# Optimization experiments

Measured on AMD Instinct MI355X. Metric: run time of the kernel, lower is better.

Reference implementation:

```python
import jax, jax.numpy as jnp
import numpy as np

N_NODES = 100000
N_EDGES = 3200000
D_IN = 96      # sum(latent_dim)
D_OUT = 32     # latent_dim[-1]
N_HEADS = 4
LEAKY_SLOPE = 0.2


def setup_inputs() -> dict:
    key = jax.random.key(0)
    k_x, k_w, k_a, k_src, k_dst = jax.random.split(key, 5)
    x = jax.random.normal(k_x, (N_NODES, D_IN), dtype=jnp.float32)
    # per-head GAT params (xavier-ish scale)
    W = jax.random.normal(k_w, (N_HEADS, D_IN, D_OUT), dtype=jnp.float32) * (1.414 / np.sqrt(D_IN))
    a = jax.random.normal(k_a, (N_HEADS, 2 * D_OUT), dtype=jnp.float32) * 0.1
    edge_src = jax.random.randint(k_src, (N_EDGES,), 0, N_NODES)
    edge_dst = jax.random.randint(k_dst, (N_EDGES,), 0, N_NODES)
    return {"x": x, "W": W, "a": a, "edge_src": edge_src, "edge_dst": edge_dst}


def reference(x, W, a, edge_src, edge_dst):
    # Multi-head sparse GAT layer (SpGraphAttentionLayer, concat=True, eval mode).
    N = x.shape[0]
    n_heads, _, d_out = W.shape
    outs = []
    for i in range(n_heads):  # small fixed head loop; data dims fully vectorized
        h = x @ W[i]                                   # [N, d_out]
        # a @ cat(h[src], h[dst]) == h[src]@a1 + h[dst]@a2 (avoids [E, 2*d_out] concat)
        s = h[edge_src] @ a[i, :d_out] + h[edge_dst] @ a[i, d_out:]   # [E]
        edge_e = jnp.exp(-jax.nn.leaky_relu(s, LEAKY_SLOPE))          # [E]
        # sparse_coo(edge, edge_e, [N,N]) @ h  ==  scatter-add of edge_e * h[dst] into src
        msg = edge_e[:, None] * h[edge_dst]                           # [E, d_out]
        h_prime = jax.ops.segment_sum(msg, edge_src, num_segments=N)  # [N, d_out]
        outs.append(jax.nn.elu(h_prime))
    return jnp.concatenate(outs, axis=1)  # [N, n_heads * d_out]
```

## Files before the change

kernel.cpp:

```cpp
#include <hip/hip_runtime.h>
#include <hip/hip_bf16.h>

#define DIN 96
#define DOUT 32
#define NH 4
#define DTOT 128
#define SLOPE 0.2f
#define NPBF 64
#define BSH 7
#define BNODES 128
#define MAXB 1024
#define EPB 4096
#define BCAP 5632
#define QSL  2304
#define SLSZ 2432

__device__ __forceinline__ unsigned int packbf2(float lo, float hi) {
    unsigned int a = __float_as_uint(lo), b = __float_as_uint(hi);
    a += 0x7fffu + ((a >> 16) & 1u);
    b += 0x7fffu + ((b >> 16) & 1u);
    return (a >> 16) | (b & 0xffff0000u);
}

__global__ __launch_bounds__(256) void feat_kernel(
    const float* __restrict__ x, const float* __restrict__ W,
    const float* __restrict__ a,
    unsigned int* __restrict__ hq,
    float2* __restrict__ usrc, float2* __restrict__ vdst,
    int n_nodes)
{
    __shared__ float Wlo[DIN * 64];
    __shared__ float Whi[DIN * 64];
    __shared__ float al[NH * 2 * DOUT];
    const int t = threadIdx.x;

    for (int i = t; i < DIN * DTOT; i += 256) {
        int k = i >> 7, c = i & 127;
        int head = c >> 5, j = c & 31;
        float w = W[head * (DIN * DOUT) + k * DOUT + j];
        int cbi = c >> 3, jj = c & 7;
        if (jj < 4) Wlo[(k << 6) + (cbi << 2) + jj] = w;
        else        Whi[(k << 6) + (cbi << 2) + (jj - 4)] = w;
    }
    for (int i = t; i < NH * 2 * DOUT; i += 256) al[i] = a[i];
    __syncthreads();

    const int cbi = t & 15;
    const int ng = t >> 4;
    const int node0 = blockIdx.x * NPBF;
    const int g0 = node0 + ng * 4;

    bool ok[4];
    const float* xp[4];
#pragma unroll
    for (int i = 0; i < 4; ++i) {
        ok[i] = (g0 + i) < n_nodes;
        xp[i] = x + (size_t)(g0 + i) * DIN;
    }

    float acc[4][8];
#pragma unroll
    for (int i = 0; i < 4; ++i)
#pragma unroll
        for (int j = 0; j < 8; ++j) acc[i][j] = 0.f;

    for (int k = 0; k < DIN; k += 4) {
        float4 xv[4];
#pragma unroll
        for (int i = 0; i < 4; ++i)
            xv[i] = ok[i] ? *(const float4*)(xp[i] + k)
                          : make_float4(0.f, 0.f, 0.f, 0.f);
#pragma unroll
        for (int kk = 0; kk < 4; ++kk) {
            const float4 wlo = *(const float4*)&Wlo[((k + kk) << 6) + (cbi << 2)];
            const float4 whi = *(const float4*)&Whi[((k + kk) << 6) + (cbi << 2)];
#pragma unroll
            for (int i = 0; i < 4; ++i) {
                const float xvv = (kk == 0) ? xv[i].x : (kk == 1) ? xv[i].y
                                 : (kk == 2) ? xv[i].z : xv[i].w;
                acc[i][0] = fmaf(xvv, wlo.x, acc[i][0]);
                acc[i][1] = fmaf(xvv, wlo.y, acc[i][1]);
                acc[i][2] = fmaf(xvv, wlo.z, acc[i][2]);
                acc[i][3] = fmaf(xvv, wlo.w, acc[i][3]);
                acc[i][4] = fmaf(xvv, whi.x, acc[i][4]);
                acc[i][5] = fmaf(xvv, whi.y, acc[i][5]);
                acc[i][6] = fmaf(xvv, whi.z, acc[i][6]);
                acc[i][7] = fmaf(xvv, whi.w, acc[i][7]);
            }
        }
    }

    const int head = cbi >> 2;
    const int j0 = (cbi & 3) << 3;
#pragma unroll
    for (int i = 0; i < 4; ++i) {
        float ps = 0.f, pd = 0.f;
#pragma unroll
        for (int j = 0; j < 8; ++j) {
            ps += acc[i][j] * al[head * 64 + j0 + j];
            pd += acc[i][j] * al[head * 64 + 32 + j0 + j];
        }
        ps += __shfl_xor(ps, 1); ps += __shfl_xor(ps, 2);
        pd += __shfl_xor(pd, 1); pd += __shfl_xor(pd, 2);
        const int g = g0 + i;
        if (ok[i]) {
            uint4 pk;
            pk.x = packbf2(acc[i][0], acc[i][1]);
            pk.y = packbf2(acc[i][2], acc[i][3]);
            pk.z = packbf2(acc[i][4], acc[i][5]);
            pk.w = packbf2(acc[i][6], acc[i][7]);
            *(uint4*)&hq[(size_t)g * 64 + (cbi << 2)] = pk;
            if ((cbi & 3) == 0) {
                usrc[g * NH + head] = make_float2(__expf(-ps), __expf(-SLOPE * ps));
                vdst[g * NH + head] = make_float2(__expf(-pd), __expf(-SLOPE * pd));
            }
        }
    }
}

__global__ __launch_bounds__(256) void binscatter_kernel(
    const int* __restrict__ esrc, const int* __restrict__ edst,
    int* __restrict__ gcur0, unsigned int* __restrict__ binned,
    int n_edges, int nb)
{
    __shared__ int bc[MAXB];
    const int t = threadIdx.x;
    for (int i = t; i < nb; i += 256) bc[i] = 0;
    __syncthreads();

    const int base = blockIdx.x * EPB;
    const int end = min(base + EPB, n_edges);
    const bool full = (end - base) == EPB;

    int se[16], de[16];
    if (full) {
        const int4* s4p = (const int4*)(esrc + base);
        const int4* d4p = (const int4*)(edst + base);
#pragma unroll
        for (int j = 0; j < 4; ++j) {
            int4 s4 = s4p[j * 256 + t];
            int4 d4 = d4p[j * 256 + t];
            se[j * 4 + 0] = s4.x; se[j * 4 + 1] = s4.y;
            se[j * 4 + 2] = s4.z; se[j * 4 + 3] = s4.w;
            de[j * 4 + 0] = d4.x; de[j * 4 + 1] = d4.y;
            de[j * 4 + 2] = d4.z; de[j * 4 + 3] = d4.w;
        }
#pragma unroll
        for (int j = 0; j < 16; ++j)
            atomicAdd(&bc[se[j] >> BSH], 1);
    } else {
#pragma unroll
        for (int j = 0; j < 16; ++j) {
            const int e = base + j * 256 + t;
            se[j] = (e < end) ? esrc[e] : 0;
            de[j] = (e < end) ? edst[e] : 0;
            if (e < end) atomicAdd(&bc[se[j] >> BSH], 1);
        }
    }
    __syncthreads();

    for (int i = t; i < nb; i += 256) {
        int c = bc[i];
        bc[i] = (c > 0) ? (i * BCAP + atomicAdd(&gcur0[i], c)) : 0;
    }
    __syncthreads();

    if (full) {
#pragma unroll
        for (int j = 0; j < 16; ++j) {
            int s = se[j];
            int pos = atomicAdd(&bc[s >> BSH], 1);
            binned[pos] = ((unsigned int)(s & (BNODES - 1)) << 17) | (unsigned int)de[j];
        }
    } else {
#pragma unroll
        for (int j = 0; j < 16; ++j) {
            const int e = base + j * 256 + t;
            if (e < end) {
                int s = se[j];
                int pos = atomicAdd(&bc[s >> BSH], 1);
                binned[pos] = ((unsigned int)(s & (BNODES - 1)) << 17) | (unsigned int)de[j];
            }
        }
    }
}

__global__ __launch_bounds__(512) void bucket_kernel(
    const int* __restrict__ gcur0,
    const unsigned int* __restrict__ binned,
    const unsigned int* __restrict__ hv,
    const float2* __restrict__ usrc, const float2* __restrict__ vdst,
    float* __restrict__ out, int n_nodes)
{
    __shared__ unsigned int wbuf[QSL];
    __shared__ __align__(16) int slist[SLSZ];
    __shared__ int dcnt[32];
    __shared__ int sc[32];
    __shared__ int dcur[32];
    __shared__ int qn_s;
    const int t = threadIdx.x;
    const int p = (int)blockIdx.x >> 2;
    const int q = (int)blockIdx.x & 3;
    const unsigned pbase = (unsigned)p * BCAP;
    int cnt = gcur0[p];
    if (cnt > BCAP - 512) cnt = BCAP - 512;
    const int node0 = (p << BSH) + (q << 5);

    if (t < 32) dcnt[t] = 0;
    if (t == 0) qn_s = 0;
    __syncthreads();

    for (int i = t; i < cnt; i += 512) {
        unsigned int w = binned[pbase + i];
        int s = (int)(w >> 17);
        if ((s >> 5) == q) {
            int pos = atomicAdd(&qn_s, 1);
            if (pos < QSL) {
                wbuf[pos] = w;
                atomicAdd(&dcnt[s & 31], 1);
            }
        }
    }
    __syncthreads();
    int qn = qn_s; if (qn > QSL) qn = QSL;

    int pd = 0;
    if (t < 32) { pd = (dcnt[t] + 3) & ~3; sc[t] = pd; }
    __syncthreads();
    for (int off = 1; off < 32; off <<= 1) {
        int v = 0;
        if (t < 32 && t >= off) v = sc[t - off];
        __syncthreads();
        if (t < 32) sc[t] += v;
        __syncthreads();
    }
    if (t < 32) dcur[t] = sc[t] - pd;
    __syncthreads();
    for (int i = t; i < qn; i += 512) {
        unsigned int w = wbuf[i];
        int pos = atomicAdd(&dcur[(w >> 17) & 31], 1);
        slist[pos] = (int)(w & 0x1ffffu);
    }
    __syncthreads();

    const int l = t & 63;
    const int head = l >> 4;
    const unsigned loff = (unsigned)l << 2;
    const unsigned hoff = (unsigned)head << 3;
    const char* __restrict__ hvb = (const char*)hv;
    const char* __restrict__ vdb = (const char*)vdst;
    const int sub = t >> 6;

#define LDV(c) (*(const float2*)(vdb + ((((unsigned)(c)) << 5) + hoff)))
#define LDW(c) (*(const unsigned int*)(hvb + ((((unsigned)(c)) << 8) + loff)))
#define COMP(vv, ww, AX, AY) do {                                   \
        float e_ = fminf(u.x * (vv).x, u.y * (vv).y);               \
        AX = fmaf(e_, __uint_as_float((ww) << 16), AX);             \
        AY = fmaf(e_, __uint_as_float((ww) & 0xffff0000u), AY);     \
    } while (0)

    for (int r = 0; r < 4; ++r) {
        const int nd = r * 8 + sub;
        const int node = node0 + nd;
        if (node >= n_nodes) break;
        const int d = dcnt[nd];
        const int beg = dcur[nd] - d;
        const float2 u = usrc[(unsigned)node * 4u + head];

        float ax0 = 0.f, ay0 = 0.f, ax1 = 0.f, ay1 = 0.f;
        float ax2 = 0.f, ay2 = 0.f, ax3 = 0.f, ay3 = 0.f;
        int k = 0;
        if (d >= 4) {
            int4 cA = *(const int4*)&slist[beg];
            float2 vA0 = LDV(cA.x), vA1 = LDV(cA.y), vA2 = LDV(cA.z), vA3 = LDV(cA.w);
            unsigned wA0 = LDW(cA.x), wA1 = LDW(cA.y), wA2 = LDW(cA.z), wA3 = LDW(cA.w);

            for (; k + 12 <= d; k += 8) {
                int4 cB = *(const int4*)&slist[beg + k + 4];
                float2 vB0 = LDV(cB.x), vB1 = LDV(cB.y), vB2 = LDV(cB.z), vB3 = LDV(cB.w);
                unsigned wB0 = LDW(cB.x), wB1 = LDW(cB.y), wB2 = LDW(cB.z), wB3 = LDW(cB.w);
                COMP(vA0, wA0, ax0, ay0); COMP(vA1, wA1, ax1, ay1);
                COMP(vA2, wA2, ax2, ay2); COMP(vA3, wA3, ax3, ay3);
                int4 cN = *(const int4*)&slist[beg + k + 8];
                vA0 = LDV(cN.x); vA1 = LDV(cN.y); vA2 = LDV(cN.z); vA3 = LDV(cN.w);
                wA0 = LDW(cN.x); wA1 = LDW(cN.y); wA2 = LDW(cN.z); wA3 = LDW(cN.w);
                COMP(vB0, wB0, ax0, ay0); COMP(vB1, wB1, ax1, ay1);
                COMP(vB2, wB2, ax2, ay2); COMP(vB3, wB3, ax3, ay3);
            }
            if (k + 8 <= d) {
                int4 cB = *(const int4*)&slist[beg + k + 4];
                float2 vB0 = LDV(cB.x), vB1 = LDV(cB.y), vB2 = LDV(cB.z), vB3 = LDV(cB.w);
                unsigned wB0 = LDW(cB.x), wB1 = LDW(cB.y), wB2 = LDW(cB.z), wB3 = LDW(cB.w);
                COMP(vA0, wA0, ax0, ay0); COMP(vA1, wA1, ax1, ay1);
                COMP(vA2, wA2, ax2, ay2); COMP(vA3, wA3, ax3, ay3);
                COMP(vB0, wB0, ax0, ay0); COMP(vB1, wB1, ax1, ay1);
                COMP(vB2, wB2, ax2, ay2); COMP(vB3, wB3, ax3, ay3);
                k += 8;
            } else {
                COMP(vA0, wA0, ax0, ay0); COMP(vA1, wA1, ax1, ay1);
                COMP(vA2, wA2, ax2, ay2); COMP(vA3, wA3, ax3, ay3);
                k += 4;
            }
        }
        for (; k < d; ++k) {
            int c = slist[beg + k];
            float2 v = LDV(c);
            unsigned w = LDW(c);
            COMP(v, w, ax0, ay0);
        }
        float rx = (ax0 + ax1) + (ax2 + ax3);
        float ry = (ay0 + ay1) + (ay2 + ay3);
        rx = rx > 0.f ? rx : __expf(rx) - 1.f;
        ry = ry > 0.f ? ry : __expf(ry) - 1.f;
        ((float2*)out)[(unsigned)node * 64u + l] = make_float2(rx, ry);
    }
#undef LDV
#undef LDW
#undef COMP
}

extern "C" void kernel_launch(void* const* d_in, const int* in_sizes, int n_in,
                              void* d_out, int out_size, void* d_ws, size_t ws_size,
                              hipStream_t stream)
{
    const float* x  = (const float*)d_in[0];
    const float* W  = (const float*)d_in[1];
    const float* a  = (const float*)d_in[2];
    const int* esrc = (const int*)d_in[3];
    const int* edst = (const int*)d_in[4];
    const int n_nodes = in_sizes[0] / DIN;
    const int n_edges = in_sizes[3];
    float* out = (float*)d_out;

    const int nb = (n_nodes + BNODES - 1) >> BSH;

    unsigned int* hq = (unsigned int*)d_ws;
    float2* usrc = (float2*)(hq + (size_t)n_nodes * 64);
    float2* vdst = usrc + (size_t)n_nodes * NH;
    int* gcur0  = (int*)(vdst + (size_t)n_nodes * NH);
    unsigned int* binned = (unsigned int*)(gcur0 + MAXB);

    hipMemsetAsync(gcur0, 0, MAXB * sizeof(int), stream);

    feat_kernel<<<(n_nodes + NPBF - 1) / NPBF, 256, 0, stream>>>(
        x, W, a, hq, usrc, vdst, n_nodes);

    binscatter_kernel<<<(n_edges + EPB - 1) / EPB, 256, 0, stream>>>(
        esrc, edst, gcur0, binned, n_edges, nb);

    bucket_kernel<<<nb * 4, 512, 0, stream>>>(
        gcur0, binned, hq, usrc, vdst, out, n_nodes);
}
```

Baseline: 413.1 us.

## Split feature GEMM across head halves and pad bin counters to avoid contention

The feature kernel now gives each block two of the four heads for 128 nodes, so the W tile in shared memory is halved and each thread computes 8 columns for 4 nodes. This cuts LDS use per block and may raise occupancy, but x is now read twice from global memory. Separately, the per-bin global cursors are strided 16 ints apart so each counter sits on its own cache line, which is meant to reduce false sharing between atomics. The cost is a larger memset and workspace.

```diff
diff --git a/kernel.cpp b/kernel.cpp
--- a/kernel.cpp
+++ b/kernel.cpp
@@ -6,7 +6,7 @@
 #define NH 4
 #define DTOT 128
 #define SLOPE 0.2f
-#define NPBF 64
+#define NPBF 128
 #define BSH 7
 #define BNODES 128
 #define MAXB 1024
@@ -14,6 +14,7 @@
 #define BCAP 5632
 #define QSL  2304
 #define SLSZ 2432
+#define GSTR 16
 
 __device__ __forceinline__ unsigned int packbf2(float lo, float hi) {
     unsigned int a = __float_as_uint(lo), b = __float_as_uint(hi);
@@ -29,25 +30,27 @@
     float2* __restrict__ usrc, float2* __restrict__ vdst,
     int n_nodes)
 {
-    __shared__ float Wlo[DIN * 64];
-    __shared__ float Whi[DIN * 64];
+    __shared__ float Wlo[DIN * 32];
+    __shared__ float Whi[DIN * 32];
     __shared__ float al[NH * 2 * DOUT];
     const int t = threadIdx.x;
-
-    for (int i = t; i < DIN * DTOT; i += 256) {
-        int k = i >> 7, c = i & 127;
-        int head = c >> 5, j = c & 31;
-        float w = W[head * (DIN * DOUT) + k * DOUT + j];
+    const int half = (int)blockIdx.x & 1;
+    const int nodeblk = (int)blockIdx.x >> 1;
+
+    for (int i = t; i < DIN * 64; i += 256) {
+        int k = i >> 6, c = i & 63;
+        int hl = c >> 5, j = c & 31;
+        float w = W[(half * 2 + hl) * (DIN * DOUT) + k * DOUT + j];
         int cbi = c >> 3, jj = c & 7;
-        if (jj < 4) Wlo[(k << 6) + (cbi << 2) + jj] = w;
-        else        Whi[(k << 6) + (cbi << 2) + (jj - 4)] = w;
+        if (jj < 4) Wlo[(k << 5) + (cbi << 2) + jj] = w;
+        else        Whi[(k << 5) + (cbi << 2) + (jj - 4)] = w;
     }
     for (int i = t; i < NH * 2 * DOUT; i += 256) al[i] = a[i];
     __syncthreads();
 
-    const int cbi = t & 15;
-    const int ng = t >> 4;
-    const int node0 = blockIdx.x * NPBF;
+    const int cbi = t & 7;
+    const int ng = t >> 3;
+    const int node0 = nodeblk * NPBF;
     const int g0 = node0 + ng * 4;
 
     bool ok[4];
@@ -72,8 +75,8 @@
                           : make_float4(0.f, 0.f, 0.f, 0.f);
 #pragma unroll
         for (int kk = 0; kk < 4; ++kk) {
-            const float4 wlo = *(const float4*)&Wlo[((k + kk) << 6) + (cbi << 2)];
-            const float4 whi = *(const float4*)&Whi[((k + kk) << 6) + (cbi << 2)];
+            const float4 wlo = *(const float4*)&Wlo[((k + kk) << 5) + (cbi << 2)];
+            const float4 whi = *(const float4*)&Whi[((k + kk) << 5) + (cbi << 2)];
 #pragma unroll
             for (int i = 0; i < 4; ++i) {
                 const float xvv = (kk == 0) ? xv[i].x : (kk == 1) ? xv[i].y
@@ -90,7 +93,7 @@
         }
     }
 
-    const int head = cbi >> 2;
+    const int head = half * 2 + (cbi >> 2);
     const int j0 = (cbi & 3) << 3;
 #pragma unroll
     for (int i = 0; i < 4; ++i) {
@@ -109,7 +112,7 @@
             pk.y = packbf2(acc[i][2], acc[i][3]);
             pk.z = packbf2(acc[i][4], acc[i][5]);
             pk.w = packbf2(acc[i][6], acc[i][7]);
-            *(uint4*)&hq[(size_t)g * 64 + (cbi << 2)] = pk;
+            *(uint4*)&hq[(size_t)g * 64 + half * 32 + (cbi << 2)] = pk;
             if ((cbi & 3) == 0) {
                 usrc[g * NH + head] = make_float2(__expf(-ps), __expf(-SLOPE * ps));
                 vdst[g * NH + head] = make_float2(__expf(-pd), __expf(-SLOPE * pd));
@@ -120,7 +123,7 @@
 
 __global__ __launch_bounds__(256) void binscatter_kernel(
     const int* __restrict__ esrc, const int* __restrict__ edst,
-    int* __restrict__ gcur0, unsigned int* __restrict__ binned,
+    int* __restrict__ gcur, unsigned int* __restrict__ binned,
     int n_edges, int nb)
 {
     __shared__ int bc[MAXB];
@@ -161,7 +164,7 @@
 
     for (int i = t; i < nb; i += 256) {
         int c = bc[i];
-        bc[i] = (c > 0) ? (i * BCAP + atomicAdd(&gcur0[i], c)) : 0;
+        bc[i] = (c > 0) ? (i * BCAP + atomicAdd(&gcur[i * GSTR], c)) : 0;
     }
     __syncthreads();
 
@@ -186,7 +189,7 @@
 }
 
 __global__ __launch_bounds__(512) void bucket_kernel(
-    const int* __restrict__ gcur0,
+    const int* __restrict__ gcur,
     const unsigned int* __restrict__ binned,
     const unsigned int* __restrict__ hv,
     const float2* __restrict__ usrc, const float2* __restrict__ vdst,
@@ -202,7 +205,7 @@
     const int p = (int)blockIdx.x >> 2;
     const int q = (int)blockIdx.x & 3;
     const unsigned pbase = (unsigned)p * BCAP;
-    int cnt = gcur0[p];
+    int cnt = gcur[p * GSTR];
     if (cnt > BCAP - 512) cnt = BCAP - 512;
     const int node0 = (p << BSH) + (q << 5);
 
@@ -337,17 +340,18 @@
     unsigned int* hq = (unsigned int*)d_ws;
     float2* usrc = (float2*)(hq + (size_t)n_nodes * 64);
     float2* vdst = usrc + (size_t)n_nodes * NH;
-    int* gcur0  = (int*)(vdst + (size_t)n_nodes * NH);
-    unsigned int* binned = (unsigned int*)(gcur0 + MAXB);
-
-    hipMemsetAsync(gcur0, 0, MAXB * sizeof(int), stream);
-
-    feat_kernel<<<(n_nodes + NPBF - 1) / NPBF, 256, 0, stream>>>(
+    int* gcur   = (int*)(vdst + (size_t)n_nodes * NH);
+    unsigned int* binned = (unsigned int*)(gcur + MAXB * GSTR);
+
+    hipMemsetAsync(gcur, 0, MAXB * GSTR * sizeof(int), stream);
+
+    const int nodeblks = (n_nodes + NPBF - 1) / NPBF;
+    feat_kernel<<<nodeblks * 2, 256, 0, stream>>>(
         x, W, a, hq, usrc, vdst, n_nodes);
 
     binscatter_kernel<<<(n_edges + EPB - 1) / EPB, 256, 0, stream>>>(
-        esrc, edst, gcur0, binned, n_edges, nb);
+        esrc, edst, gcur, binned, n_edges, nb);
 
     bucket_kernel<<<nb * 4, 512, 0, stream>>>(
-        gcur0, binned, hq, usrc, vdst, out, n_nodes);
-}
+        gcur, binned, hq, usrc, vdst, out, n_nodes);
+}
```

New measurement: 404.7 us. 2.0% less time.
